# Performance work log

Hardware: AMD Instinct MI355X
Metric: run time of the kernel (lower is better)

The kernel has to match this reference:

```python
import jax, jax.numpy as jnp
import numpy as np

N = 100000
E = 1600000
IN_CH, HID_CH, OUT_CH = 128, 64, 32


def setup_inputs() -> dict:
    key = jax.random.key(0)
    ks = jax.random.split(key, 6)
    x = jax.random.normal(ks[0], (N, IN_CH), dtype=jnp.float32)
    ei = jax.random.randint(ks[1], (2, E), 0, N, dtype=jnp.int64)
    W1 = jax.random.normal(ks[2], (IN_CH, HID_CH), dtype=jnp.float32) * 0.05
    b1 = jax.random.normal(ks[3], (HID_CH,), dtype=jnp.float32) * 0.05
    W2 = jax.random.normal(ks[4], (HID_CH, OUT_CH), dtype=jnp.float32) * 0.05
    b2 = jax.random.normal(ks[5], (OUT_CH,), dtype=jnp.float32) * 0.05
    return {"x": x, "ei": ei, "W1": W1, "b1": b1, "W2": W2, "b2": b2}


def gcn_layer(x, sa, da, n):
    # degree with self-loops already appended in sa/da
    deg = jax.ops.segment_sum(jnp.ones((sa.shape[0],), x.dtype), da, num_segments=n)
    prod = deg[sa] * deg[da]
    norm = jnp.where(prod > 0, jax.lax.rsqrt(prod), 0.0)  # (deg_s*deg_d)^-0.5, inf->0
    msg = x[sa] * norm[:, None]            # [E+N, C] gather + scale
    return jax.ops.segment_sum(msg, da, num_segments=n)  # scatter_add


def reference(x, ei, W1, b1, W2, b2):
    n = x.shape[0]
    loop = jnp.arange(n, dtype=ei.dtype)
    sa = jnp.concatenate([ei[0], loop])
    da = jnp.concatenate([ei[1], loop])
    h = gcn_layer(x @ W1 + b1, sa, da, n)
    h = jax.nn.relu(h)
    # dropout: eval mode (training=False) -> identity
    return gcn_layer(h @ W2 + b2, sa, da, n)
```

## Files before the change

### kernel.cpp

```cpp
#include <hip/hip_runtime.h>

#define NN 100000
#define NE 1600000
#define IN_CH 128
#define HID_CH 64
#define OUT_CH 32
#define NBUCK 391
#define CHUNKA 8192

typedef unsigned short ushort_t;

__device__ inline ushort_t f2bf(float f) {
    union { float f; unsigned u; } v; v.f = f;
    unsigned r = v.u + 0x7fff + ((v.u >> 16) & 1);
    return (ushort_t)(r >> 16);
}
__device__ inline float bf2f(ushort_t h) {
    union { unsigned u; float f; } v; v.u = ((unsigned)h) << 16;
    return v.f;
}

__global__ __launch_bounds__(256) void k_bhist(const int* __restrict__ da,
                                               int* __restrict__ bcnt) {
    __shared__ int hist[NBUCK];
    int t = threadIdx.x;
    for (int i = t; i < NBUCK; i += 256) hist[i] = 0;
    __syncthreads();
    int base = blockIdx.x * CHUNKA;
    for (int i = 0; i < CHUNKA; i += 256) {
        int e = base + i + t;
        if (e < NE) atomicAdd(&hist[da[e] >> 8], 1);
    }
    __syncthreads();
    for (int i = t; i < NBUCK; i += 256) {
        int c = hist[i];
        if (c) atomicAdd(&bcnt[i], c);
    }
}

__global__ __launch_bounds__(512) void k_bscan(const int* __restrict__ bcnt,
                                               int* __restrict__ bbase,
                                               int* __restrict__ bcur,
                                               int* __restrict__ rowptr) {
    __shared__ int lds[512];
    int t = threadIdx.x;
    int v = (t < NBUCK) ? bcnt[t] : 0;
    lds[t] = v;
    __syncthreads();
    for (int off = 1; off < 512; off <<= 1) {
        int x = (t >= off) ? lds[t - off] : 0;
        __syncthreads();
        lds[t] += x;
        __syncthreads();
    }
    int excl = lds[t] - v;
    if (t < NBUCK) { bbase[t] = excl; bcur[t] = excl; }
    if (t == 0) { bbase[NBUCK] = NE; rowptr[NN] = NE; }
}

__global__ __launch_bounds__(256) void k_bfill(const int* __restrict__ sa,
                                               const int* __restrict__ da,
                                               int* __restrict__ bcur,
                                               unsigned* __restrict__ ebuf) {
    __shared__ int hist[NBUCK];
    __shared__ int lcur[NBUCK];
    int t = threadIdx.x;
    for (int i = t; i < NBUCK; i += 256) hist[i] = 0;
    __syncthreads();
    int base = blockIdx.x * CHUNKA;
    for (int i = 0; i < CHUNKA; i += 256) {
        int e = base + i + t;
        if (e < NE) atomicAdd(&hist[da[e] >> 8], 1);
    }
    __syncthreads();
    for (int b = t; b < NBUCK; b += 256) {
        int c = hist[b];
        lcur[b] = c ? atomicAdd(&bcur[b], c) : 0;
    }
    __syncthreads();
    for (int i = 0; i < CHUNKA; i += 256) {
        int e = base + i + t;
        if (e < NE) {
            int d = da[e];
            int p = atomicAdd(&lcur[d >> 8], 1);
            ebuf[p] = ((unsigned)sa[e] << 8) | (unsigned)(d & 255);
        }
    }
}

__global__ __launch_bounds__(256) void k_bfine(const unsigned* __restrict__ ebuf,
                                               const int* __restrict__ bbase,
                                               int* __restrict__ rowptr,
                                               float* __restrict__ rs,
                                               int* __restrict__ col) {
    __shared__ int cnt[256];
    __shared__ int cur[256];
    __shared__ int scn[256];
    int b = blockIdx.x, t = threadIdx.x;
    int nb = NN - b * 256; if (nb > 256) nb = 256;
    int beg = bbase[b], end = bbase[b + 1];
    cnt[t] = 0;
    __syncthreads();
    for (int i = beg + t; i < end; i += 256) atomicAdd(&cnt[ebuf[i] & 255], 1);
    __syncthreads();
    int v = cnt[t];
    scn[t] = v;
    __syncthreads();
    for (int off = 1; off < 256; off <<= 1) {
        int x = (t >= off) ? scn[t - off] : 0;
        __syncthreads();
        scn[t] += x;
        __syncthreads();
    }
    int excl = scn[t] - v;
    if (t < nb) {
        rowptr[b * 256 + t] = beg + excl;
        rs[b * 256 + t] = rsqrtf((float)(v + 1));
        cur[t] = beg + excl;
    }
    __syncthreads();
    for (int i = beg + t; i < end; i += 256) {
        unsigned p = ebuf[i];
        int pos = atomicAdd(&cur[p & 255], 1);
        col[pos] = (int)(p >> 8);
    }
}

#define SWZ1(n, k) ((n) * 128 + ((k) ^ ((((n) & 7)) << 2)))
#define SWZ2(n, k) ((n) * 64 + ((k) ^ ((((n) & 7)) << 2)))

__global__ __launch_bounds__(256) void k_gemm1(
    const float* __restrict__ x, const float* __restrict__ W1,
    const float* __restrict__ b1, const float* __restrict__ rs,
    ushort_t* __restrict__ xsb) {
    __shared__ float xt[64 * 128];
    __shared__ float w1s[128 * 64];
    int t = threadIdx.x;
    int base = blockIdx.x * 64;

#pragma unroll
    for (int i = 0; i < 8; ++i) {
        int flat = i * 1024 + t * 4;
        int node = flat >> 7, k0 = flat & 127;
        int gn = base + node;
        float4 v = make_float4(0.f, 0.f, 0.f, 0.f);
        if (gn < NN) v = *(const float4*)(x + (size_t)gn * IN_CH + k0);
        *(float4*)&xt[SWZ1(node, k0)] = v;
        *(float4*)&w1s[flat] = *(const float4*)(W1 + flat);
    }
    __syncthreads();

    int tn = t & 15, tc = t >> 4;
    int c0 = tc * 4;
    float acc[4][4];
#pragma unroll
    for (int a = 0; a < 4; ++a)
#pragma unroll
        for (int b = 0; b < 4; ++b) acc[a][b] = 0.f;

    for (int k0 = 0; k0 < 128; k0 += 4) {
        float xq[4][4], wq[4][4];
#pragma unroll
        for (int j = 0; j < 4; ++j)
            *(float4*)&wq[j][0] = *(float4*)&w1s[(k0 + j) * 64 + c0];
#pragma unroll
        for (int jn = 0; jn < 4; ++jn)
            *(float4*)&xq[jn][0] = *(float4*)&xt[SWZ1(tn + jn * 16, k0)];
#pragma unroll
        for (int jn = 0; jn < 4; ++jn)
#pragma unroll
            for (int j = 0; j < 4; ++j)
#pragma unroll
                for (int jc = 0; jc < 4; ++jc)
                    acc[jn][jc] = fmaf(xq[jn][j], wq[j][jc], acc[jn][jc]);
    }

    float4 bb = *(const float4*)&b1[c0];
#pragma unroll
    for (int jn = 0; jn < 4; ++jn) {
        int gn = base + tn + jn * 16;
        if (gn < NN) {
            float r = rs[gn];
            uint2 pk;
            pk.x = (unsigned)f2bf((acc[jn][0] + bb.x) * r) |
                   ((unsigned)f2bf((acc[jn][1] + bb.y) * r) << 16);
            pk.y = (unsigned)f2bf((acc[jn][2] + bb.z) * r) |
                   ((unsigned)f2bf((acc[jn][3] + bb.w) * r) << 16);
            *(uint2*)&xsb[(size_t)gn * HID_CH + c0] = pk;
        }
    }
}

__global__ void k_agg1(const int* __restrict__ rowptr, const int* __restrict__ col,
                       const ushort_t* __restrict__ xsb, const float* __restrict__ rs,
                       float* __restrict__ h) {
    int gid = blockIdx.x * blockDim.x + threadIdx.x;
    int n = gid >> 6;
    int c = gid & 63;
    if (n >= NN) return;
    int beg = rowptr[n], end = rowptr[n + 1];
    float acc = bf2f(xsb[n * HID_CH + c]);
    int i = beg;
    for (; i + 3 < end; i += 4) {
        int s0 = col[i], s1 = col[i + 1], s2 = col[i + 2], s3 = col[i + 3];
        acc += bf2f(xsb[s0 * HID_CH + c]);
        acc += bf2f(xsb[s1 * HID_CH + c]);
        acc += bf2f(xsb[s2 * HID_CH + c]);
        acc += bf2f(xsb[s3 * HID_CH + c]);
    }
    for (; i < end; ++i) acc += bf2f(xsb[col[i] * HID_CH + c]);
    h[n * HID_CH + c] = fmaxf(acc * rs[n], 0.f);
}

__global__ __launch_bounds__(256) void k_gemm2(
    const float* __restrict__ h, const float* __restrict__ W2,
    const float* __restrict__ b2, const float* __restrict__ rs,
    ushort_t* __restrict__ ysb) {
    __shared__ float ht[64 * 64];
    __shared__ float w2s[64 * 32];
    int t = threadIdx.x;
    int base = blockIdx.x * 64;

#pragma unroll
    for (int i = 0; i < 4; ++i) {
        int flat = i * 1024 + t * 4;
        int node = flat >> 6, k0 = flat & 63;
        int gn = base + node;
        float4 v = make_float4(0.f, 0.f, 0.f, 0.f);
        if (gn < NN) v = *(const float4*)(h + (size_t)gn * HID_CH + k0);
        *(float4*)&ht[SWZ2(node, k0)] = v;
    }
#pragma unroll
    for (int i = 0; i < 2; ++i) {
        int flat = i * 1024 + t * 4;
        *(float4*)&w2s[flat] = *(const float4*)(W2 + flat);
    }
    __syncthreads();

    int tn = t & 15, tc = t >> 4;
    int c0 = tc * 2;
    float acc[4][2];
#pragma unroll
    for (int a = 0; a < 4; ++a) { acc[a][0] = 0.f; acc[a][1] = 0.f; }

    for (int k0 = 0; k0 < 64; k0 += 4) {
        float xq[4][4], wq[4][2];
#pragma unroll
        for (int j = 0; j < 4; ++j)
            *(float2*)&wq[j][0] = *(float2*)&w2s[(k0 + j) * 32 + c0];
#pragma unroll
        for (int jn = 0; jn < 4; ++jn)
            *(float4*)&xq[jn][0] = *(float4*)&ht[SWZ2(tn + jn * 16, k0)];
#pragma unroll
        for (int jn = 0; jn < 4; ++jn)
#pragma unroll
            for (int j = 0; j < 4; ++j) {
                acc[jn][0] = fmaf(xq[jn][j], wq[j][0], acc[jn][0]);
                acc[jn][1] = fmaf(xq[jn][j], wq[j][1], acc[jn][1]);
            }
    }

    float2 bb = *(const float2*)&b2[c0];
#pragma unroll
    for (int jn = 0; jn < 4; ++jn) {
        int gn = base + tn + jn * 16;
        if (gn < NN) {
            float r = rs[gn];
            unsigned pk = (unsigned)f2bf((acc[jn][0] + bb.x) * r) |
                          ((unsigned)f2bf((acc[jn][1] + bb.y) * r) << 16);
            *(unsigned*)&ysb[(size_t)gn * OUT_CH + c0] = pk;
        }
    }
}

__global__ void k_agg2(const int* __restrict__ rowptr, const int* __restrict__ col,
                       const ushort_t* __restrict__ ysb, const float* __restrict__ rs,
                       float* __restrict__ out) {
    int gid = blockIdx.x * blockDim.x + threadIdx.x;
    int n = gid >> 5;
    int c = gid & 31;
    if (n >= NN) return;
    int beg = rowptr[n], end = rowptr[n + 1];
    float acc = bf2f(ysb[n * OUT_CH + c]);
    int i = beg;
    for (; i + 3 < end; i += 4) {
        int s0 = col[i], s1 = col[i + 1], s2 = col[i + 2], s3 = col[i + 3];
        acc += bf2f(ysb[s0 * OUT_CH + c]);
        acc += bf2f(ysb[s1 * OUT_CH + c]);
        acc += bf2f(ysb[s2 * OUT_CH + c]);
        acc += bf2f(ysb[s3 * OUT_CH + c]);
    }
    for (; i < end; ++i) acc += bf2f(ysb[col[i] * OUT_CH + c]);
    out[n * OUT_CH + c] = acc * rs[n];
}

extern "C" void kernel_launch(void* const* d_in, const int* in_sizes, int n_in,
                              void* d_out, int out_size, void* d_ws, size_t ws_size,
                              hipStream_t stream) {
    const float* x  = (const float*)d_in[0];
    const int*   ei = (const int*)d_in[1];
    const float* W1 = (const float*)d_in[2];
    const float* b1 = (const float*)d_in[3];
    const float* W2 = (const float*)d_in[4];
    const float* b2 = (const float*)d_in[5];
    const int* sa = ei;
    const int* da = ei + NE;

    char* ws = (char*)d_ws;
    size_t off = 0;
    auto alloc = [&](size_t bytes) {
        void* p = ws + off;
        off += (bytes + 255) & ~(size_t)255;
        return p;
    };
    int*      bcnt   = (int*)alloc((size_t)NBUCK * 4);
    int*      bbase  = (int*)alloc((size_t)(NBUCK + 1) * 4);
    int*      bcur   = (int*)alloc((size_t)NBUCK * 4);
    int*      rowptr = (int*)alloc((size_t)(NN + 1) * 4);
    float*    rs     = (float*)alloc((size_t)NN * 4);
    unsigned* ebuf   = (unsigned*)alloc((size_t)NE * 4);
    int*      col    = (int*)alloc((size_t)NE * 4);
    ushort_t* xsb    = (ushort_t*)alloc((size_t)NN * HID_CH * 2);
    float*    hbuf   = (float*)alloc((size_t)NN * HID_CH * 4);
    ushort_t* ysb    = xsb;
    float*    outp   = (float*)d_out;

    const int B = 256;
    const int NBLKA = (NE + CHUNKA - 1) / CHUNKA;
    hipMemsetAsync(bcnt, 0, (size_t)NBUCK * 4, stream);
    k_bhist<<<NBLKA, 256, 0, stream>>>(da, bcnt);
    k_bscan<<<1, 512, 0, stream>>>(bcnt, bbase, bcur, rowptr);
    k_bfill<<<NBLKA, 256, 0, stream>>>(sa, da, bcur, ebuf);
    k_bfine<<<NBUCK, 256, 0, stream>>>(ebuf, bbase, rowptr, rs, col);

    const int NBLK_GEMM = (NN + 63) / 64;
    k_gemm1<<<NBLK_GEMM, 256, 0, stream>>>(x, W1, b1, rs, xsb);
    k_agg1<<<(NN * 64 + B - 1) / B, B, 0, stream>>>(rowptr, col, xsb, rs, hbuf);
    k_gemm2<<<NBLK_GEMM, 256, 0, stream>>>(hbuf, W2, b2, rs, ysb);
    k_agg2<<<(NN * 32 + B - 1) / B, B, 0, stream>>>(rowptr, col, ysb, rs, outp);
}
```

Before: 242.5 us.

## Vectorize aggregation gathers and split edges across lane groups with shuffle reduction

The two aggregation kernels now give each wavefront one node. Lanes are split into groups that each handle a different neighbour edge and load 4 bf16 channels per lane with 8-byte loads. Partial sums are combined with xor shuffles. The aim is fewer, wider gather instructions and more independent edge loads in flight per node, in exchange for shuffle overhead and idle lanes on low-degree tails; agg2 also launches twice as many threads.

After: 222.6 us. 1.09x faster.

```diff
diff --git a/kernel.cpp b/kernel.cpp
--- a/kernel.cpp
+++ b/kernel.cpp
@@ -15,9 +15,11 @@
     unsigned r = v.u + 0x7fff + ((v.u >> 16) & 1);
     return (ushort_t)(r >> 16);
 }
-__device__ inline float bf2f(ushort_t h) {
-    union { unsigned u; float f; } v; v.u = ((unsigned)h) << 16;
-    return v.f;
+__device__ inline float blo(unsigned u) {
+    union { unsigned x; float f; } v; v.x = u << 16; return v.f;
+}
+__device__ inline float bhi(unsigned u) {
+    union { unsigned x; float f; } v; v.x = u & 0xffff0000u; return v.f;
 }
 
 __global__ __launch_bounds__(256) void k_bhist(const int* __restrict__ da,
@@ -191,25 +193,60 @@
     }
 }
 
-__global__ void k_agg1(const int* __restrict__ rowptr, const int* __restrict__ col,
-                       const ushort_t* __restrict__ xsb, const float* __restrict__ rs,
-                       float* __restrict__ h) {
+__global__ __launch_bounds__(256) void k_agg1(
+    const int* __restrict__ rowptr, const int* __restrict__ col,
+    const ushort_t* __restrict__ xsb, const float* __restrict__ rs,
+    float* __restrict__ h) {
     int gid = blockIdx.x * blockDim.x + threadIdx.x;
     int n = gid >> 6;
-    int c = gid & 63;
     if (n >= NN) return;
+    int lane = threadIdx.x & 63;
+    int g = lane >> 4;
+    unsigned c0 = (unsigned)(lane & 15) * 4;
     int beg = rowptr[n], end = rowptr[n + 1];
-    float acc = bf2f(xsb[n * HID_CH + c]);
+
+    float a0 = 0.f, a1 = 0.f, a2 = 0.f, a3 = 0.f;
+    if (g == 0) {
+        uint2 sv = *(const uint2*)&xsb[(unsigned)n * 64u + c0];
+        a0 = blo(sv.x); a1 = bhi(sv.x); a2 = blo(sv.y); a3 = bhi(sv.y);
+    }
+
     int i = beg;
-    for (; i + 3 < end; i += 4) {
-        int s0 = col[i], s1 = col[i + 1], s2 = col[i + 2], s3 = col[i + 3];
-        acc += bf2f(xsb[s0 * HID_CH + c]);
-        acc += bf2f(xsb[s1 * HID_CH + c]);
-        acc += bf2f(xsb[s2 * HID_CH + c]);
-        acc += bf2f(xsb[s3 * HID_CH + c]);
-    }
-    for (; i < end; ++i) acc += bf2f(xsb[col[i] * HID_CH + c]);
-    h[n * HID_CH + c] = fmaxf(acc * rs[n], 0.f);
+    for (; i + 8 <= end; i += 8) {
+        int s0 = col[i + g];
+        int s1 = col[i + 4 + g];
+        uint2 v0 = *(const uint2*)&xsb[(unsigned)s0 * 64u + c0];
+        uint2 v1 = *(const uint2*)&xsb[(unsigned)s1 * 64u + c0];
+        a0 += blo(v0.x); a1 += bhi(v0.x); a2 += blo(v0.y); a3 += bhi(v0.y);
+        a0 += blo(v1.x); a1 += bhi(v1.x); a2 += blo(v1.y); a3 += bhi(v1.y);
+    }
+    if (i + 4 <= end) {
+        int s0 = col[i + g];
+        uint2 v0 = *(const uint2*)&xsb[(unsigned)s0 * 64u + c0];
+        a0 += blo(v0.x); a1 += bhi(v0.x); a2 += blo(v0.y); a3 += bhi(v0.y);
+        i += 4;
+    }
+    int r = end - i;
+    if (g < r) {
+        int s0 = col[i + g];
+        uint2 v0 = *(const uint2*)&xsb[(unsigned)s0 * 64u + c0];
+        a0 += blo(v0.x); a1 += bhi(v0.x); a2 += blo(v0.y); a3 += bhi(v0.y);
+    }
+
+    a0 += __shfl_xor(a0, 16); a1 += __shfl_xor(a1, 16);
+    a2 += __shfl_xor(a2, 16); a3 += __shfl_xor(a3, 16);
+    a0 += __shfl_xor(a0, 32); a1 += __shfl_xor(a1, 32);
+    a2 += __shfl_xor(a2, 32); a3 += __shfl_xor(a3, 32);
+
+    if (g == 0) {
+        float rn = rs[n];
+        float4 o;
+        o.x = fmaxf(a0 * rn, 0.f);
+        o.y = fmaxf(a1 * rn, 0.f);
+        o.z = fmaxf(a2 * rn, 0.f);
+        o.w = fmaxf(a3 * rn, 0.f);
+        *(float4*)&h[(size_t)n * HID_CH + c0] = o;
+    }
 }
 
 __global__ __launch_bounds__(256) void k_gemm2(
@@ -273,25 +310,59 @@
     }
 }
 
-__global__ void k_agg2(const int* __restrict__ rowptr, const int* __restrict__ col,
-                       const ushort_t* __restrict__ ysb, const float* __restrict__ rs,
-                       float* __restrict__ out) {
+__global__ __launch_bounds__(256) void k_agg2(
+    const int* __restrict__ rowptr, const int* __restrict__ col,
+    const ushort_t* __restrict__ ysb, const float* __restrict__ rs,
+    float* __restrict__ out) {
     int gid = blockIdx.x * blockDim.x + threadIdx.x;
-    int n = gid >> 5;
-    int c = gid & 31;
+    int n = gid >> 6;
     if (n >= NN) return;
+    int lane = threadIdx.x & 63;
+    int g = lane >> 3;
+    unsigned c0 = (unsigned)(lane & 7) * 4;
     int beg = rowptr[n], end = rowptr[n + 1];
-    float acc = bf2f(ysb[n * OUT_CH + c]);
+
+    float a0 = 0.f, a1 = 0.f, a2 = 0.f, a3 = 0.f;
+    if (g == 0) {
+        uint2 sv = *(const uint2*)&ysb[(unsigned)n * 32u + c0];
+        a0 = blo(sv.x); a1 = bhi(sv.x); a2 = blo(sv.y); a3 = bhi(sv.y);
+    }
+
     int i = beg;
-    for (; i + 3 < end; i += 4) {
-        int s0 = col[i], s1 = col[i + 1], s2 = col[i + 2], s3 = col[i + 3];
-        acc += bf2f(ysb[s0 * OUT_CH + c]);
-        acc += bf2f(ysb[s1 * OUT_CH + c]);
-        acc += bf2f(ysb[s2 * OUT_CH + c]);
-        acc += bf2f(ysb[s3 * OUT_CH + c]);
-    }
-    for (; i < end; ++i) acc += bf2f(ysb[col[i] * OUT_CH + c]);
-    out[n * OUT_CH + c] = acc * rs[n];
+    for (; i + 16 <= end; i += 16) {
+        int s0 = col[i + g];
+        int s1 = col[i + 8 + g];
+        uint2 v0 = *(const uint2*)&ysb[(unsigned)s0 * 32u + c0];
+        uint2 v1 = *(const uint2*)&ysb[(unsigned)s1 * 32u + c0];
+        a0 += blo(v0.x); a1 += bhi(v0.x); a2 += blo(v0.y); a3 += bhi(v0.y);
+        a0 += blo(v1.x); a1 += bhi(v1.x); a2 += blo(v1.y); a3 += bhi(v1.y);
+    }
+    if (i + 8 <= end) {
+        int s0 = col[i + g];
+        uint2 v0 = *(const uint2*)&ysb[(unsigned)s0 * 32u + c0];
+        a0 += blo(v0.x); a1 += bhi(v0.x); a2 += blo(v0.y); a3 += bhi(v0.y);
+        i += 8;
+    }
+    int r = end - i;
+    if (g < r) {
+        int s0 = col[i + g];
+        uint2 v0 = *(const uint2*)&ysb[(unsigned)s0 * 32u + c0];
+        a0 += blo(v0.x); a1 += bhi(v0.x); a2 += blo(v0.y); a3 += bhi(v0.y);
+    }
+
+    a0 += __shfl_xor(a0, 8);  a1 += __shfl_xor(a1, 8);
+    a2 += __shfl_xor(a2, 8);  a3 += __shfl_xor(a3, 8);
+    a0 += __shfl_xor(a0, 16); a1 += __shfl_xor(a1, 16);
+    a2 += __shfl_xor(a2, 16); a3 += __shfl_xor(a3, 16);
+    a0 += __shfl_xor(a0, 32); a1 += __shfl_xor(a1, 32);
+    a2 += __shfl_xor(a2, 32); a3 += __shfl_xor(a3, 32);
+
+    if (g == 0) {
+        float rn = rs[n];
+        float4 o;
+        o.x = a0 * rn; o.y = a1 * rn; o.z = a2 * rn; o.w = a3 * rn;
+        *(float4*)&out[(size_t)n * OUT_CH + c0] = o;
+    }
 }
 
 extern "C" void kernel_launch(void* const* d_in, const int* in_sizes, int n_in,
@@ -337,5 +408,5 @@
     k_gemm1<<<NBLK_GEMM, 256, 0, stream>>>(x, W1, b1, rs, xsb);
     k_agg1<<<(NN * 64 + B - 1) / B, B, 0, stream>>>(rowptr, col, xsb, rs, hbuf);
     k_gemm2<<<NBLK_GEMM, 256, 0, stream>>>(hbuf, W2, b2, rs, ysb);
-    k_agg2<<<(NN * 32 + B - 1) / B, B, 0, stream>>>(rowptr, col, ysb, rs, outp);
-}
+    k_agg2<<<(NN * 64 + B - 1) / B, B, 0, stream>>>(rowptr, col, ysb, rs, outp);
+}
```
